# Kernel optimization log

Hardware: AMD Instinct MI355X
Metric: run time of the kernel (lower is better)

Reference implementation:

```python
import jax, jax.numpy as jnp
import numpy as np

B, S, D, H = 2, 2048, 1024, 16
DK = D // H


def setup_inputs() -> dict:
    key = jax.random.key(0)
    ks = jax.random.split(key, 7)
    return {
        "query": jax.random.normal(ks[0], (B, S, D), jnp.float32),
        "key": jax.random.normal(ks[1], (B, S, D), jnp.float32),
        "value": jax.random.normal(ks[2], (B, S, D), jnp.float32),
        "w_q": jax.random.normal(ks[3], (D, D), jnp.float32) * (1.0 / np.sqrt(D)),
        "w_k": jax.random.normal(ks[4], (D, D), jnp.float32) * (1.0 / np.sqrt(D)),
        "w_v": jax.random.normal(ks[5], (D, D), jnp.float32) * (1.0 / np.sqrt(D)),
        "w_o": jax.random.normal(ks[6], (D, D), jnp.float32) * (1.0 / np.sqrt(D)),
    }


def reference(query, key, value, w_q, w_k, w_v, w_o):
    # Linear(bias=False) in torch computes x @ W.T where W is [out, in].
    Q = jnp.einsum('bsd,ed->bse', query, w_q)
    K = jnp.einsum('bsd,ed->bse', key, w_k)
    V = jnp.einsum('bsd,ed->bse', value, w_v)
    # split heads: [B, H, S, DK]
    Q = Q.reshape(B, S, H, DK).transpose(0, 2, 1, 3)
    K = K.reshape(B, S, H, DK).transpose(0, 2, 1, 3)
    V = V.reshape(B, S, H, DK).transpose(0, 2, 1, 3)
    scale = 1.0 / np.sqrt(DK).astype(np.float32)
    scores = jnp.einsum('bhqd,bhkd->bhqk', Q, K) * scale  # [B,H,S,S]
    attn = jax.nn.softmax(scores, axis=-1)
    context = jnp.einsum('bhqk,bhkd->bhqd', attn, V)
    context = context.transpose(0, 2, 1, 3).reshape(B, S, D)
    return jnp.einsum('bsd,ed->bse', context, w_o)
```

## Files before the change

kernel.cpp:

```cpp
#include <hip/hip_runtime.h>

typedef unsigned short u16;
typedef unsigned int u32;
typedef __bf16 bf16x8 __attribute__((ext_vector_type(8)));
typedef float f32x4 __attribute__((ext_vector_type(4)));
typedef short s16x4 __attribute__((ext_vector_type(4)));

#define AS1 __attribute__((address_space(1)))
#define AS3 __attribute__((address_space(3)))

__device__ __forceinline__ f32x4 mfma16(bf16x8 a, bf16x8 b, f32x4 c) {
    return __builtin_amdgcn_mfma_f32_16x16x32_bf16(a, b, c, 0, 0, 0);
}
__device__ __forceinline__ f32x4 mfma16k16(s16x4 a, s16x4 b, f32x4 c) {
    return __builtin_amdgcn_mfma_f32_16x16x16bf16_1k(a, b, c, 0, 0, 0);
}

__device__ __forceinline__ u16 f2bf(float f) {
    return __builtin_bit_cast(u16, (__bf16)f);
}

__device__ __forceinline__ void gld16(const u16* g, u16* l) {
    __builtin_amdgcn_global_load_lds((AS1 void*)g, (AS3 void*)l, 16, 0, 0);
}

__global__ __launch_bounds__(256) void cvt_all(const float* __restrict__ q, const float* __restrict__ k,
                                               const float* __restrict__ v, const float* __restrict__ wq,
                                               const float* __restrict__ wk, const float* __restrict__ wv,
                                               const float* __restrict__ wo, u16* __restrict__ qo,
                                               u16* __restrict__ ko, u16* __restrict__ vo,
                                               u16* __restrict__ wqo, u16* __restrict__ wko,
                                               u16* __restrict__ wvo, u16* __restrict__ woo) {
    const int y = blockIdx.y;
    const float* x; u16* o; int n;
    switch (y) {
        case 0: x = q; o = qo; n = 4 << 20; break;
        case 1: x = k; o = ko; n = 4 << 20; break;
        case 2: x = v; o = vo; n = 4 << 20; break;
        case 3: x = wq; o = wqo; n = 1 << 20; break;
        case 4: x = wk; o = wko; n = 1 << 20; break;
        case 5: x = wv; o = wvo; n = 1 << 20; break;
        default: x = wo; o = woo; n = 1 << 20; break;
    }
    int i = (blockIdx.x * 256 + threadIdx.x) * 4;
    if (i >= n) return;
    float4 vv = *(const float4*)(x + i);
    u32 lo = (u32)f2bf(vv.x) | ((u32)f2bf(vv.y) << 16);
    u32 hi = (u32)f2bf(vv.z) | ((u32)f2bf(vv.w) << 16);
    *(uint2*)(o + i) = make_uint2(lo, hi);
}

template <bool BF16OUT>
__device__ __forceinline__ void gemm_core(const u16* __restrict__ A, const u16* __restrict__ Bt,
                                          void* __restrict__ Cp, int K, int N, int m0, int n0,
                                          float oscale) {
    __shared__ __align__(16) u16 As[128 * 32];
    __shared__ __align__(16) u16 Bs[128 * 32];
    const int tid = threadIdx.x;
    const int lane = tid & 63, wave = tid >> 6;
    const int l16 = lane & 15, q4 = lane >> 4;
    const int wm = (wave >> 1) * 64, wn = (wave & 1) * 64;

    const f32x4 fz = {0.f, 0.f, 0.f, 0.f};
    f32x4 acc[4][4];
#pragma unroll
    for (int i = 0; i < 4; ++i)
#pragma unroll
        for (int j = 0; j < 4; ++j) acc[i][j] = fz;

    const int rseg = lane >> 2;
    const int ck = ((lane & 3) ^ ((lane >> 3) & 3)) * 8;
    const int r0 = wave * 16 + rseg, r1 = r0 + 64;
    const u16* Ag0 = A + (size_t)(m0 + r0) * K + ck;
    const u16* Ag1 = A + (size_t)(m0 + r1) * K + ck;
    const u16* Bg0 = Bt + (size_t)(n0 + r0) * K + ck;
    const u16* Bg1 = Bt + (size_t)(n0 + r1) * K + ck;
    u16* As0 = As + wave * 512;
    u16* As1 = As + (wave + 4) * 512;
    u16* Bs0 = Bs + wave * 512;
    u16* Bs1 = Bs + (wave + 4) * 512;

    const int swz = (q4 ^ ((l16 & 7) >> 1)) * 8;

    for (int k0 = 0; k0 < K; k0 += 32) {
        __syncthreads();
        gld16(Ag0 + k0, As0);
        gld16(Ag1 + k0, As1);
        gld16(Bg0 + k0, Bs0);
        gld16(Bg1 + k0, Bs1);
        __syncthreads();
        bf16x8 af[4], bfr[4];
#pragma unroll
        for (int i = 0; i < 4; ++i)
            af[i] = *(const bf16x8*)&As[(wm + i * 16 + l16) * 32 + swz];
#pragma unroll
        for (int j = 0; j < 4; ++j)
            bfr[j] = *(const bf16x8*)&Bs[(wn + j * 16 + l16) * 32 + swz];
#pragma unroll
        for (int i = 0; i < 4; ++i)
#pragma unroll
            for (int j = 0; j < 4; ++j) acc[i][j] = mfma16(af[i], bfr[j], acc[i][j]);
    }

#pragma unroll
    for (int i = 0; i < 4; ++i) {
        const int row = m0 + wm + i * 16 + q4 * 4;
#pragma unroll
        for (int j = 0; j < 4; ++j) {
            const int col = n0 + wn + j * 16 + l16;
#pragma unroll
            for (int r = 0; r < 4; ++r) {
                const float vr = acc[i][j][r] * oscale;
                if constexpr (BF16OUT)
                    ((u16*)Cp)[(size_t)(row + r) * N + col] = f2bf(vr);
                else
                    ((float*)Cp)[(size_t)(row + r) * N + col] = vr;
            }
        }
    }
}

__global__ __launch_bounds__(256) void gemm_qkv(const u16* __restrict__ qb, const u16* __restrict__ kb,
                                                const u16* __restrict__ vb, const u16* __restrict__ wqb,
                                                const u16* __restrict__ wkb, const u16* __restrict__ wvb,
                                                u16* __restrict__ Qp, u16* __restrict__ Kp,
                                                u16* __restrict__ VtAll) {
    const int z = blockIdx.y, x = blockIdx.x;
    const u16 *A, *Bt;
    u16* C;
    int N, m0, n0;
    float sc = 1.0f;
    if (z == 0) {
        A = qb; Bt = wqb; C = Qp; N = 1024; m0 = (x >> 3) * 128; n0 = (x & 7) * 128;
        sc = 0.18033688011112042f;
    } else if (z == 1) {
        A = kb; Bt = wkb; C = Kp; N = 1024; m0 = (x >> 3) * 128; n0 = (x & 7) * 128;
    } else {
        A = wvb; Bt = vb; C = VtAll; N = 4096; m0 = (x >> 5) * 128; n0 = (x & 31) * 128;
    }
    gemm_core<true>(A, Bt, C, 1024, N, m0, n0, sc);
}

__global__ __launch_bounds__(256) void gemm_out(const u16* __restrict__ ctx,
                                                const u16* __restrict__ wob,
                                                float* __restrict__ out) {
    const int x = blockIdx.x;
    gemm_core<false>(ctx, wob, out, 1024, 1024, (x >> 3) * 128, (x & 7) * 128, 1.0f);
}

__global__ __launch_bounds__(256) void flash_attn(const u16* __restrict__ Qp,
                                                  const u16* __restrict__ Kp,
                                                  const u16* __restrict__ VtAll,
                                                  u16* __restrict__ Ctx) {
    constexpr int D = 1024, SS = 2048, LD = 72;
    __shared__ __align__(16) u16 Ks[64 * LD];
    __shared__ __align__(16) u16 Vts[64 * LD];

    const int tid = threadIdx.x;
    const int lane = tid & 63, wave = tid >> 6;
    const int l16 = lane & 15, q4 = lane >> 4;
    const int h = blockIdx.y, b = blockIdx.z;
    const int q0 = blockIdx.x * 128 + wave * 32;

    bf16x8 qf[2][2];
#pragma unroll
    for (int qs = 0; qs < 2; ++qs) {
        const u16* Qb = Qp + (size_t)(b * SS + q0 + qs * 16 + l16) * D + h * 64;
        qf[qs][0] = *(const bf16x8*)(Qb + q4 * 8);
        qf[qs][1] = *(const bf16x8*)(Qb + 32 + q4 * 8);
    }

    const f32x4 fz = {0.f, 0.f, 0.f, 0.f};
    f32x4 ot[2][4];
    float lsum[2] = {0.f, 0.f};
#pragma unroll
    for (int qs = 0; qs < 2; ++qs)
#pragma unroll
        for (int dt = 0; dt < 4; ++dt) ot[qs][dt] = fz;

    const int sr = tid >> 3, scol = (tid & 7) * 8;
    const u16* Kg = Kp + (size_t)(b * SS + sr) * D + h * 64 + scol;
    const u16* Vg = VtAll + (size_t)(h * 64 + sr) * 4096 + b * SS + scol;

    uint4 k0v = *(const uint4*)(Kg);
    uint4 k1v = *(const uint4*)(Kg + (size_t)32 * D);
    uint4 v0v = *(const uint4*)(Vg);
    uint4 v1v = *(const uint4*)(Vg + (size_t)32 * 4096);

    for (int kt = 0; kt < SS; kt += 64) {
        __syncthreads();
        *(uint4*)&Ks[sr * LD + scol] = k0v;
        *(uint4*)&Ks[(sr + 32) * LD + scol] = k1v;
        *(uint4*)&Vts[sr * LD + scol] = v0v;
        *(uint4*)&Vts[(sr + 32) * LD + scol] = v1v;
        __syncthreads();

        const int nk = (kt + 64 < SS) ? kt + 64 : 0;
        k0v = *(const uint4*)(Kg + (size_t)nk * D);
        k1v = *(const uint4*)(Kg + (size_t)(nk + 32) * D);
        v0v = *(const uint4*)(Vg + nk);
        v1v = *(const uint4*)(Vg + (size_t)32 * 4096 + nk);

        f32x4 st[2][4];
#pragma unroll
        for (int nt = 0; nt < 4; ++nt) {
            const bf16x8 ka = *(const bf16x8*)&Ks[(nt * 16 + l16) * LD + q4 * 8];
            const bf16x8 kb = *(const bf16x8*)&Ks[(nt * 16 + l16) * LD + 32 + q4 * 8];
#pragma unroll
            for (int qs = 0; qs < 2; ++qs) {
                f32x4 s = mfma16(ka, qf[qs][0], fz);
                st[qs][nt] = mfma16(kb, qf[qs][1], s);
            }
        }
        s16x4 p[2][4];
#pragma unroll
        for (int qs = 0; qs < 2; ++qs)
#pragma unroll
            for (int nt = 0; nt < 4; ++nt) {
                const float e0 = __builtin_amdgcn_exp2f(st[qs][nt][0]);
                const float e1 = __builtin_amdgcn_exp2f(st[qs][nt][1]);
                const float e2 = __builtin_amdgcn_exp2f(st[qs][nt][2]);
                const float e3 = __builtin_amdgcn_exp2f(st[qs][nt][3]);
                lsum[qs] += (e0 + e1) + (e2 + e3);
                s16x4 pk;
                pk[0] = (short)f2bf(e0);
                pk[1] = (short)f2bf(e1);
                pk[2] = (short)f2bf(e2);
                pk[3] = (short)f2bf(e3);
                p[qs][nt] = pk;
            }
#pragma unroll
        for (int nt = 0; nt < 4; ++nt)
#pragma unroll
            for (int dt = 0; dt < 4; ++dt) {
                const s16x4 va = *(const s16x4*)&Vts[(dt * 16 + l16) * LD + nt * 16 + q4 * 4];
#pragma unroll
                for (int qs = 0; qs < 2; ++qs)
                    ot[qs][dt] = mfma16k16(va, p[qs][nt], ot[qs][dt]);
            }
    }

#pragma unroll
    for (int qs = 0; qs < 2; ++qs) {
        lsum[qs] += __shfl_xor(lsum[qs], 16, 64);
        lsum[qs] += __shfl_xor(lsum[qs], 32, 64);
        lsum[qs] = 1.f / lsum[qs];
    }

#pragma unroll
    for (int qs = 0; qs < 2; ++qs) {
        u16* Cb = Ctx + (size_t)(b * SS + q0 + qs * 16 + l16) * D + h * 64 + q4 * 4;
#pragma unroll
        for (int dt = 0; dt < 4; ++dt) {
            s16x4 w;
#pragma unroll
            for (int r = 0; r < 4; ++r) w[r] = (short)f2bf(ot[qs][dt][r] * lsum[qs]);
            *(s16x4*)(Cb + dt * 16) = w;
        }
    }
}

extern "C" void kernel_launch(void* const* d_in, const int* in_sizes, int n_in,
                              void* d_out, int out_size, void* d_ws, size_t ws_size,
                              hipStream_t stream) {
    const float* query = (const float*)d_in[0];
    const float* key   = (const float*)d_in[1];
    const float* value = (const float*)d_in[2];
    const float* w_q   = (const float*)d_in[3];
    const float* w_k   = (const float*)d_in[4];
    const float* w_v   = (const float*)d_in[5];
    const float* w_o   = (const float*)d_in[6];
    float* out = (float*)d_out;

    const size_t MEG = 1024 * 1024;
    if (ws_size < 64 * MEG) return;
    u16* ws = (u16*)d_ws;
    u16* qb    = ws;
    u16* kb    = ws + 4 * MEG;
    u16* vb    = ws + 8 * MEG;
    u16* wqb   = ws + 12 * MEG;
    u16* wkb   = ws + 13 * MEG;
    u16* wvb   = ws + 14 * MEG;
    u16* wob   = ws + 15 * MEG;
    u16* Qp    = ws + 16 * MEG;
    u16* Kp    = ws + 20 * MEG;
    u16* VtAll = ws + 24 * MEG;
    u16* ctx   = ws + 28 * MEG;

    cvt_all<<<dim3(4096, 7), 256, 0, stream>>>(query, key, value, w_q, w_k, w_v, w_o,
                                               qb, kb, vb, wqb, wkb, wvb, wob);
    gemm_qkv<<<dim3(256, 3), 256, 0, stream>>>(qb, kb, vb, wqb, wkb, wvb, Qp, Kp, VtAll);
    flash_attn<<<dim3(16, 16, 2), 256, 0, stream>>>(Qp, Kp, VtAll, ctx);
    gemm_out<<<dim3(256), 256, 0, stream>>>(ctx, wob, out);
}
```

Before: 227.1 us.

## Split attention over key range with combine kernel, smaller out-projection tiles

Flash attention now splits the key sequence into NS chunks (two when the workspace is large enough), giving twice the blocks. Each split writes unnormalized fp32 partial outputs and row sums, and a new combine kernel adds them, normalizes and converts to bf16. Row sums are now computed with an MFMA against a ones vector instead of scalar adds and shuffles, and the V tile in LDS gets an XOR swizzle to reduce bank conflicts. The output GEMM uses 64x128 tiles, doubling its block count. The cost is an extra kernel launch plus fp32 partial-output traffic, and the partial buffers reuse workspace regions that earlier stages have finished with.

```diff
diff --git a/kernel.cpp b/kernel.cpp
--- a/kernel.cpp
+++ b/kernel.cpp
@@ -50,63 +50,61 @@
     *(uint2*)(o + i) = make_uint2(lo, hi);
 }
 
-template <bool BF16OUT>
+template <int BM, int BN, bool BF16OUT>
 __device__ __forceinline__ void gemm_core(const u16* __restrict__ A, const u16* __restrict__ Bt,
                                           void* __restrict__ Cp, int K, int N, int m0, int n0,
                                           float oscale) {
-    __shared__ __align__(16) u16 As[128 * 32];
-    __shared__ __align__(16) u16 Bs[128 * 32];
+    constexpr int WROWS = BM / 64;
+    constexpr int WCOLS = 4 / WROWS;
+    constexpr int BFR = BN / WCOLS / 16;
+    __shared__ __align__(16) u16 As[BM * 32];
+    __shared__ __align__(16) u16 Bs[BN * 32];
     const int tid = threadIdx.x;
     const int lane = tid & 63, wave = tid >> 6;
     const int l16 = lane & 15, q4 = lane >> 4;
-    const int wm = (wave >> 1) * 64, wn = (wave & 1) * 64;
+    const int wm = (wave / WCOLS) * 64, wn = (wave % WCOLS) * (BFR * 16);
 
     const f32x4 fz = {0.f, 0.f, 0.f, 0.f};
-    f32x4 acc[4][4];
+    f32x4 acc[4][BFR];
 #pragma unroll
     for (int i = 0; i < 4; ++i)
 #pragma unroll
-        for (int j = 0; j < 4; ++j) acc[i][j] = fz;
+        for (int j = 0; j < BFR; ++j) acc[i][j] = fz;
 
     const int rseg = lane >> 2;
     const int ck = ((lane & 3) ^ ((lane >> 3) & 3)) * 8;
-    const int r0 = wave * 16 + rseg, r1 = r0 + 64;
-    const u16* Ag0 = A + (size_t)(m0 + r0) * K + ck;
-    const u16* Ag1 = A + (size_t)(m0 + r1) * K + ck;
-    const u16* Bg0 = Bt + (size_t)(n0 + r0) * K + ck;
-    const u16* Bg1 = Bt + (size_t)(n0 + r1) * K + ck;
-    u16* As0 = As + wave * 512;
-    u16* As1 = As + (wave + 4) * 512;
-    u16* Bs0 = Bs + wave * 512;
-    u16* Bs1 = Bs + (wave + 4) * 512;
+    const u16* Ag = A + (size_t)(m0 + wave * 16 + rseg) * K + ck;
+    const u16* Bg = Bt + (size_t)(n0 + wave * 16 + rseg) * K + ck;
 
     const int swz = (q4 ^ ((l16 & 7) >> 1)) * 8;
 
     for (int k0 = 0; k0 < K; k0 += 32) {
         __syncthreads();
-        gld16(Ag0 + k0, As0);
-        gld16(Ag1 + k0, As1);
-        gld16(Bg0 + k0, Bs0);
-        gld16(Bg1 + k0, Bs1);
+#pragma unroll
+        for (int p = 0; p < BM / 64; ++p)
+            gld16(Ag + (size_t)p * 64 * K + k0, As + p * 2048 + wave * 512);
+#pragma unroll
+        for (int p = 0; p < BN / 64; ++p)
+            gld16(Bg + (size_t)p * 64 * K + k0, Bs + p * 2048 + wave * 512);
         __syncthreads();
-        bf16x8 af[4], bfr[4];
+        bf16x8 af[4], bfr[BFR];
 #pragma unroll
         for (int i = 0; i < 4; ++i)
             af[i] = *(const bf16x8*)&As[(wm + i * 16 + l16) * 32 + swz];
 #pragma unroll
-        for (int j = 0; j < 4; ++j)
+        for (int j = 0; j < BFR; ++j)
             bfr[j] = *(const bf16x8*)&Bs[(wn + j * 16 + l16) * 32 + swz];
 #pragma unroll
         for (int i = 0; i < 4; ++i)
 #pragma unroll
-            for (int j = 0; j < 4; ++j) acc[i][j] = mfma16(af[i], bfr[j], acc[i][j]);
+            for (int j = 0; j < BFR; ++j) acc[i][j] = mfma16(af[i], bfr[j], acc[i][j]);
     }
 
 #pragma unroll
     for (int i = 0; i < 4; ++i) {
         const int row = m0 + wm + i * 16 + q4 * 4;
 #pragma unroll
-        for (int j = 0; j < 4; ++j) {
+        for (int j = 0; j < BFR; ++j) {
             const int col = n0 + wn + j * 16 + l16;
 #pragma unroll
             for (int r = 0; r < 4; ++r) {
@@ -138,20 +136,23 @@
     } else {
         A = wvb; Bt = vb; C = VtAll; N = 4096; m0 = (x >> 5) * 128; n0 = (x & 31) * 128;
     }
-    gemm_core<true>(A, Bt, C, 1024, N, m0, n0, sc);
+    gemm_core<128, 128, true>(A, Bt, C, 1024, N, m0, n0, sc);
 }
 
 __global__ __launch_bounds__(256) void gemm_out(const u16* __restrict__ ctx,
                                                 const u16* __restrict__ wob,
                                                 float* __restrict__ out) {
     const int x = blockIdx.x;
-    gemm_core<false>(ctx, wob, out, 1024, 1024, (x >> 3) * 128, (x & 7) * 128, 1.0f);
+    gemm_core<64, 128, false>(ctx, wob, out, 1024, 1024, (x >> 3) * 64, (x & 7) * 128, 1.0f);
 }
 
 __global__ __launch_bounds__(256) void flash_attn(const u16* __restrict__ Qp,
                                                   const u16* __restrict__ Kp,
                                                   const u16* __restrict__ VtAll,
-                                                  u16* __restrict__ Ctx) {
+                                                  float* __restrict__ Op0,
+                                                  float* __restrict__ Op1,
+                                                  float* __restrict__ Lp,
+                                                  int NS, int ktLen) {
     constexpr int D = 1024, SS = 2048, LD = 72;
     __shared__ __align__(16) u16 Ks[64 * LD];
     __shared__ __align__(16) u16 Vts[64 * LD];
@@ -159,8 +160,10 @@
     const int tid = threadIdx.x;
     const int lane = tid & 63, wave = tid >> 6;
     const int l16 = lane & 15, q4 = lane >> 4;
-    const int h = blockIdx.y, b = blockIdx.z;
+    const int h = blockIdx.y;
+    const int b = blockIdx.z / NS, half = blockIdx.z - b * NS;
     const int q0 = blockIdx.x * 128 + wave * 32;
+    const int kt0 = half * ktLen, ktEnd = kt0 + ktLen;
 
     bf16x8 qf[2][2];
 #pragma unroll
@@ -171,23 +174,32 @@
     }
 
     const f32x4 fz = {0.f, 0.f, 0.f, 0.f};
-    f32x4 ot[2][4];
-    float lsum[2] = {0.f, 0.f};
+    f32x4 ot[2][4], lacc[2];
+    lacc[0] = fz; lacc[1] = fz;
 #pragma unroll
     for (int qs = 0; qs < 2; ++qs)
 #pragma unroll
         for (int dt = 0; dt < 4; ++dt) ot[qs][dt] = fz;
 
+    s16x4 onesA;
+    onesA[0] = onesA[1] = onesA[2] = onesA[3] = (short)0x3F80;
+
     const int sr = tid >> 3, scol = (tid & 7) * 8;
+    const int vswap = wave & 1;
+    const int swV = (l16 >> 3) & 1;
     const u16* Kg = Kp + (size_t)(b * SS + sr) * D + h * 64 + scol;
     const u16* Vg = VtAll + (size_t)(h * 64 + sr) * 4096 + b * SS + scol;
 
-    uint4 k0v = *(const uint4*)(Kg);
-    uint4 k1v = *(const uint4*)(Kg + (size_t)32 * D);
-    uint4 v0v = *(const uint4*)(Vg);
-    uint4 v1v = *(const uint4*)(Vg + (size_t)32 * 4096);
-
-    for (int kt = 0; kt < SS; kt += 64) {
+    uint4 k0v = *(const uint4*)(Kg + (size_t)kt0 * D);
+    uint4 k1v = *(const uint4*)(Kg + (size_t)(kt0 + 32) * D);
+    uint4 v0v = *(const uint4*)(Vg + kt0);
+    uint4 v1v = *(const uint4*)(Vg + (size_t)32 * 4096 + kt0);
+
+    for (int kt = kt0; kt < ktEnd; kt += 64) {
+        if (vswap) {
+            v0v = make_uint4(v0v.z, v0v.w, v0v.x, v0v.y);
+            v1v = make_uint4(v1v.z, v1v.w, v1v.x, v1v.y);
+        }
         __syncthreads();
         *(uint4*)&Ks[sr * LD + scol] = k0v;
         *(uint4*)&Ks[(sr + 32) * LD + scol] = k1v;
@@ -195,7 +207,7 @@
         *(uint4*)&Vts[(sr + 32) * LD + scol] = v1v;
         __syncthreads();
 
-        const int nk = (kt + 64 < SS) ? kt + 64 : 0;
+        const int nk = (kt + 64 < ktEnd) ? kt + 64 : kt0;
         k0v = *(const uint4*)(Kg + (size_t)nk * D);
         k1v = *(const uint4*)(Kg + (size_t)(nk + 32) * D);
         v0v = *(const uint4*)(Vg + nk);
@@ -205,11 +217,11 @@
 #pragma unroll
         for (int nt = 0; nt < 4; ++nt) {
             const bf16x8 ka = *(const bf16x8*)&Ks[(nt * 16 + l16) * LD + q4 * 8];
-            const bf16x8 kb = *(const bf16x8*)&Ks[(nt * 16 + l16) * LD + 32 + q4 * 8];
+            const bf16x8 kbf = *(const bf16x8*)&Ks[(nt * 16 + l16) * LD + 32 + q4 * 8];
 #pragma unroll
             for (int qs = 0; qs < 2; ++qs) {
                 f32x4 s = mfma16(ka, qf[qs][0], fz);
-                st[qs][nt] = mfma16(kb, qf[qs][1], s);
+                st[qs][nt] = mfma16(kbf, qf[qs][1], s);
             }
         }
         s16x4 p[2][4];
@@ -217,47 +229,57 @@
         for (int qs = 0; qs < 2; ++qs)
 #pragma unroll
             for (int nt = 0; nt < 4; ++nt) {
-                const float e0 = __builtin_amdgcn_exp2f(st[qs][nt][0]);
-                const float e1 = __builtin_amdgcn_exp2f(st[qs][nt][1]);
-                const float e2 = __builtin_amdgcn_exp2f(st[qs][nt][2]);
-                const float e3 = __builtin_amdgcn_exp2f(st[qs][nt][3]);
-                lsum[qs] += (e0 + e1) + (e2 + e3);
                 s16x4 pk;
-                pk[0] = (short)f2bf(e0);
-                pk[1] = (short)f2bf(e1);
-                pk[2] = (short)f2bf(e2);
-                pk[3] = (short)f2bf(e3);
+#pragma unroll
+                for (int r = 0; r < 4; ++r)
+                    pk[r] = (short)f2bf(__builtin_amdgcn_exp2f(st[qs][nt][r]));
                 p[qs][nt] = pk;
             }
 #pragma unroll
-        for (int nt = 0; nt < 4; ++nt)
+        for (int nt = 0; nt < 4; ++nt) {
 #pragma unroll
             for (int dt = 0; dt < 4; ++dt) {
-                const s16x4 va = *(const s16x4*)&Vts[(dt * 16 + l16) * LD + nt * 16 + q4 * 4];
-#pragma unroll
-                for (int qs = 0; qs < 2; ++qs)
-                    ot[qs][dt] = mfma16k16(va, p[qs][nt], ot[qs][dt]);
+                const s16x4 va = *(const s16x4*)&Vts[(dt * 16 + l16) * LD + ((nt * 4 + q4) ^ swV) * 4];
+                ot[0][dt] = mfma16k16(va, p[0][nt], ot[0][dt]);
+                ot[1][dt] = mfma16k16(va, p[1][nt], ot[1][dt]);
             }
-    }
-
+            lacc[0] = mfma16k16(onesA, p[0][nt], lacc[0]);
+            lacc[1] = mfma16k16(onesA, p[1][nt], lacc[1]);
+        }
+    }
+
+    float* Op = half ? Op1 : Op0;
 #pragma unroll
     for (int qs = 0; qs < 2; ++qs) {
-        lsum[qs] += __shfl_xor(lsum[qs], 16, 64);
-        lsum[qs] += __shfl_xor(lsum[qs], 32, 64);
-        lsum[qs] = 1.f / lsum[qs];
-    }
-
-#pragma unroll
-    for (int qs = 0; qs < 2; ++qs) {
-        u16* Cb = Ctx + (size_t)(b * SS + q0 + qs * 16 + l16) * D + h * 64 + q4 * 4;
-#pragma unroll
-        for (int dt = 0; dt < 4; ++dt) {
-            s16x4 w;
-#pragma unroll
-            for (int r = 0; r < 4; ++r) w[r] = (short)f2bf(ot[qs][dt][r] * lsum[qs]);
-            *(s16x4*)(Cb + dt * 16) = w;
-        }
-    }
+        const int q = q0 + qs * 16 + l16;
+        float* orow = Op + (size_t)(b * SS + q) * 1024 + h * 64;
+#pragma unroll
+        for (int dt = 0; dt < 4; ++dt)
+            *(f32x4*)(orow + dt * 16 + q4 * 4) = ot[qs][dt];
+        if (lane < 16)
+            Lp[((half * 2 + b) * 16 + h) * 2048 + q] = lacc[qs][0];
+    }
+}
+
+__global__ __launch_bounds__(256) void combine(const float* __restrict__ Op0,
+                                               const float* __restrict__ Op1,
+                                               const float* __restrict__ Lp,
+                                               u16* __restrict__ ctx, int NS) {
+    const int t = blockIdx.x * 256 + threadIdx.x;
+    const int e = t * 4;
+    const int d = e & 1023, bq = e >> 10;
+    const int h = d >> 6, b = bq >> 11, q = bq & 2047;
+    f32x4 o = *(const f32x4*)(Op0 + (size_t)bq * 1024 + d);
+    float l = Lp[(b * 16 + h) * 2048 + q];
+    if (NS == 2) {
+        o += *(const f32x4*)(Op1 + (size_t)bq * 1024 + d);
+        l += Lp[((2 + b) * 16 + h) * 2048 + q];
+    }
+    const float inv = 1.f / l;
+    s16x4 w;
+#pragma unroll
+    for (int r = 0; r < 4; ++r) w[r] = (short)f2bf(o[r] * inv);
+    *(s16x4*)(ctx + (size_t)bq * 1024 + d) = w;
 }
 
 extern "C" void kernel_launch(void* const* d_in, const int* in_sizes, int n_in,
@@ -287,9 +309,17 @@
     u16* VtAll = ws + 24 * MEG;
     u16* ctx   = ws + 28 * MEG;
 
+    float* Op0 = (float*)ws;
+    float* Lp  = (float*)(ws + 12 * MEG);
+    float* Op1 = (float*)(ws + 32 * MEG);
+
+    const int NS = (ws_size >= 80 * MEG) ? 2 : 1;
+    const int ktLen = 2048 / NS;
+
     cvt_all<<<dim3(4096, 7), 256, 0, stream>>>(query, key, value, w_q, w_k, w_v, w_o,
                                                qb, kb, vb, wqb, wkb, wvb, wob);
     gemm_qkv<<<dim3(256, 3), 256, 0, stream>>>(qb, kb, vb, wqb, wkb, wvb, Qp, Kp, VtAll);
-    flash_attn<<<dim3(16, 16, 2), 256, 0, stream>>>(Qp, Kp, VtAll, ctx);
-    gemm_out<<<dim3(256), 256, 0, stream>>>(ctx, wob, out);
-}
+    flash_attn<<<dim3(16, 16, 2 * NS), 256, 0, stream>>>(Qp, Kp, VtAll, Op0, Op1, Lp, NS, ktLen);
+    combine<<<dim3(4096), 256, 0, stream>>>(Op0, Op1, Lp, ctx, NS);
+    gemm_out<<<dim3(512), 256, 0, stream>>>(ctx, wob, out);
+}
```

Measured after the change: 229.3 us. About the same (+1.0%).
